# Kernel optimization log

Hardware: AMD Instinct MI355X
Metric: run time of the kernel (lower is better)

The kernel has to match this reference:

```python
import jax, jax.numpy as jnp
import numpy as np

N_HEADS = 4
SIGMA = 6.0
T_IN = 12
T_TOTAL = 24


def setup_inputs() -> dict:
    key = jax.random.key(0)
    k1, k2, k3, k4, k5 = jax.random.split(key, 5)
    B, T, N, C, K = 16, T_IN, 5000, 4, 16
    x = jax.random.normal(k1, (B, T, N, C), dtype=jnp.float32)
    dists = jax.random.uniform(k2, (N, K), dtype=jnp.float32) * 10.0  # kNN distances
    neighbors = jax.random.randint(k3, (N, K), 0, N)                  # kNN indices
    d_in = T * N_HEADS                   # 48
    d_out = T_TOTAL - T_IN               # 12
    W = jax.random.normal(k4, (d_in, d_out), dtype=jnp.float32) * (1.0 / np.sqrt(d_in))
    b = jax.random.normal(k5, (d_out,), dtype=jnp.float32) * 0.01
    return {"x": x, "dists": dists, "W": W, "b": b, "neighbors": neighbors}


def reference(x, dists, W, b, neighbors):
    B, T, N, C = x.shape
    H = N_HEADS
    # lambda_h = h/H for h = 1..H
    lam = jnp.arange(1, H + 1, dtype=x.dtype) / H                     # [H]
    # weights[n,k,h] = exp(-d_{nk}^2 * lam_h / sigma^2)
    w = jnp.exp(-(dists ** 2)[:, :, None] * lam / (SIGMA ** 2))       # [N,K,H]
    # gather neighbor features: [B,T,N,K,C]
    xg = x[:, :, neighbors, :]
    # distance-weighted aggregation over neighbors -> [B,T,N,H,C]
    agg = jnp.einsum('btnkc,nkh->btnhc', xg, w)
    # permute (0,2,4,1,3) -> [B,N,C,T,H], flatten last two -> [B,N,C,T*H]
    feat = jnp.transpose(agg, (0, 2, 4, 1, 3)).reshape(B, N, C, T * H)
    # shrink: Linear + ReLU -> [B,N,C,T_TOTAL-T]
    y = jax.nn.relu(feat @ W + b)
    # -> [B, T_TOTAL-T, N, C]
    y = jnp.transpose(y, (0, 3, 1, 2))
    return jnp.concatenate([x, y], axis=1)                            # [B,T_TOTAL,N,C]
```

## Files before the change

### kernel.cpp

```cpp
#include <hip/hip_runtime.h>

#define Bz 16
#define Tin 12
#define Ttot 24
#define NN 5000
#define Cc 4
#define KK 16
#define HH 4
#define OO 12
#define TH 48
#define G  8
#define JJ 24

typedef float f32x4 __attribute__((ext_vector_type(4)));
__device__ __forceinline__ void nt_store4(float4* p, float4 v) {
    f32x4 t; t.x = v.x; t.y = v.y; t.z = v.z; t.w = v.w;
    __builtin_nontemporal_store(t, (f32x4*)p);
}

#define K1_NB 64
#define K1_BT 24

__global__ __launch_bounds__(256) void transpose_kernel(
    const float4* __restrict__ x4,
    float4* __restrict__ xT2)
{
    __shared__ float4 tile[K1_BT][K1_NB + 1];
    const int bid = blockIdx.x;
    const int g   = bid & 7;
    const int n0  = (bid >> 3) * K1_NB;
    const int bt0 = g * K1_BT;
    const int rem = min(K1_NB, NN - n0);
    const int tid = threadIdx.x;

    #pragma unroll
    for (int r = 0; r < (K1_NB * K1_BT) / 256; r++) {
        int tau = r * 256 + tid;
        int j = tau / K1_NB;
        int i = tau % K1_NB;
        if (i < rem)
            tile[j][i] = x4[(size_t)(bt0 + j) * NN + n0 + i];
    }
    __syncthreads();

    #pragma unroll
    for (int r = 0; r < (K1_NB * K1_BT) / 256; r++) {
        int tau = r * 256 + tid;
        int i = tau / K1_BT;
        int j = tau - i * K1_BT;
        if (i < rem)
            xT2[((size_t)g * NN + n0 + i) * JJ + j] = tile[j][i];
    }
}

#define NPB 8
#define FST 5
#define FSB 61
#define FSN 123

__global__ __launch_bounds__(192) void gnn_main_kernel(
    const float4* __restrict__ x4,
    const float4* __restrict__ xT2,
    const float* __restrict__ dists,
    const float* __restrict__ W,
    const float* __restrict__ bias,
    const int*   __restrict__ nbrs,
    float4* __restrict__ out4)
{
    __shared__ float4 feat[NPB * FSN];
    __shared__ float4 w4_s[NPB][KK];
    __shared__ float  W_s[TH * OO];
    __shared__ float  bias_s[OO];
    __shared__ int    nbr_s[NPB][KK];

    const int bid = blockIdx.x;
    const int g   = bid & 7;
    const int n0  = (bid >> 3) * NPB;
    const int tid = threadIdx.x;

    for (int i = tid; i < TH * OO; i += 192) W_s[i] = W[i];
    if (tid < OO) bias_s[tid] = bias[tid];
    if (tid < NPB * KK) {
        int nl = tid >> 4, k = tid & 15;
        nbr_s[nl][k] = nbrs[(n0 + nl) * KK + k];
        float d = dists[(n0 + nl) * KK + k];
        float e = -(d * d) * (1.0f / 144.0f);
        float4 wv;
        wv.x = expf(e);
        wv.y = expf(2.0f * e);
        wv.z = expf(3.0f * e);
        wv.w = expf(4.0f * e);
        w4_s[nl][k] = wv;
    }

    {
        const int j  = tid >> 3;
        const int nl = tid & 7;
        const int bt = g * JJ + j;
        const int b  = bt / Tin, t = bt - b * Tin;
        float4 v = x4[(size_t)bt * NN + n0 + nl];
        nt_store4(&out4[(size_t)(b * Ttot + t) * NN + n0 + nl], v);
    }
    __syncthreads();

    {
        const int nl  = tid / JJ;
        const int j   = tid - nl * JJ;
        const int b_l = j / Tin;
        const int t   = j - b_l * Tin;
        const float4* xg = xT2 + (size_t)g * NN * JJ;

        float4 a0 = {0,0,0,0}, a1 = {0,0,0,0}, a2 = {0,0,0,0}, a3 = {0,0,0,0};
        #pragma unroll
        for (int k = 0; k < KK; k++) {
            float4 xv = xg[(size_t)nbr_s[nl][k] * JJ + j];
            float4 wv = w4_s[nl][k];
            a0.x += wv.x * xv.x; a0.y += wv.x * xv.y; a0.z += wv.x * xv.z; a0.w += wv.x * xv.w;
            a1.x += wv.y * xv.x; a1.y += wv.y * xv.y; a1.z += wv.y * xv.z; a1.w += wv.y * xv.w;
            a2.x += wv.z * xv.x; a2.y += wv.z * xv.y; a2.z += wv.z * xv.z; a2.w += wv.z * xv.w;
            a3.x += wv.w * xv.x; a3.y += wv.w * xv.y; a3.z += wv.w * xv.z; a3.w += wv.w * xv.w;
        }
        const int base = nl * FSN + b_l * FSB + t * FST;
        feat[base + 0] = a0;
        feat[base + 1] = a1;
        feat[base + 2] = a2;
        feat[base + 3] = a3;
    }
    __syncthreads();

    {
        const int nl  = tid & 7;
        const int bo  = tid >> 3;
        const int b_l = bo / OO;
        const int o   = bo - b_l * OO;
        const float bz = bias_s[o];
        float4 acc = {bz, bz, bz, bz};
        const int fbase = nl * FSN + b_l * FSB;
        #pragma unroll
        for (int t = 0; t < Tin; t++) {
            #pragma unroll
            for (int h = 0; h < HH; h++) {
                float  wv = W_s[(t * HH + h) * OO + o];
                float4 f  = feat[fbase + t * FST + h];
                acc.x += wv * f.x; acc.y += wv * f.y;
                acc.z += wv * f.z; acc.w += wv * f.w;
            }
        }
        acc.x = fmaxf(acc.x, 0.0f); acc.y = fmaxf(acc.y, 0.0f);
        acc.z = fmaxf(acc.z, 0.0f); acc.w = fmaxf(acc.w, 0.0f);
        const int b = g * 2 + b_l;
        nt_store4(&out4[(size_t)(b * Ttot + Tin + o) * NN + n0 + nl], acc);
    }
}

extern "C" void kernel_launch(void* const* d_in, const int* in_sizes, int n_in,
                              void* d_out, int out_size, void* d_ws, size_t ws_size,
                              hipStream_t stream) {
    const float* x     = (const float*)d_in[0];
    const float* dists = (const float*)d_in[1];
    const float* W     = (const float*)d_in[2];
    const float* bias  = (const float*)d_in[3];
    const int*   nbrs  = (const int*)d_in[4];
    float4* out4 = (float4*)d_out;
    float4* xT2  = (float4*)d_ws;

    const int ntiles = (NN + K1_NB - 1) / K1_NB;
    hipLaunchKernelGGL(transpose_kernel, dim3(ntiles * G), dim3(256), 0, stream,
                       (const float4*)x, xT2);

    hipLaunchKernelGGL(gnn_main_kernel, dim3((NN / NPB) * G), dim3(192), 0, stream,
                       (const float4*)x, (const float4*)xT2,
                       dists, W, bias, nbrs, out4);
}
```

Measured before the change: 106.1 us.

## Fuse transpose and main pass into one persistent cooperative kernel with grid sync

```diff
diff --git a/kernel.cpp b/kernel.cpp
--- a/kernel.cpp
+++ b/kernel.cpp
@@ -1,10 +1,12 @@
 #include <hip/hip_runtime.h>
+#include <hip/hip_cooperative_groups.h>
+
+namespace cg = cooperative_groups;
 
 #define Bz 16
 #define Tin 12
 #define Ttot 24
 #define NN 5000
-#define Cc 4
 #define KK 16
 #define HH 4
 #define OO 12
@@ -12,87 +14,201 @@
 #define G  8
 #define JJ 24
 
+#define BPG 128
+#define NPB 8
+#define GPG 625
+#define TNB 40
+#define NT  125
+
+#define FST 5
+#define FSB 61
+#define FSN 122
+
+#define OFF_W4   16000
+#define OFF_NBR  18048
+#define OFF_WS   18560
+#define OFF_BIAS 20864
+#define SMEM_BYTES 20928
+
 typedef float f32x4 __attribute__((ext_vector_type(4)));
 __device__ __forceinline__ void nt_store4(float4* p, float4 v) {
     f32x4 t; t.x = v.x; t.y = v.y; t.z = v.z; t.w = v.w;
     __builtin_nontemporal_store(t, (f32x4*)p);
 }
 
-#define K1_NB 64
-#define K1_BT 24
-
-__global__ __launch_bounds__(256) void transpose_kernel(
+__global__ __launch_bounds__(256, 4) void gnn_fused_kernel(
     const float4* __restrict__ x4,
-    float4* __restrict__ xT2)
-{
-    __shared__ float4 tile[K1_BT][K1_NB + 1];
-    const int bid = blockIdx.x;
-    const int g   = bid & 7;
-    const int n0  = (bid >> 3) * K1_NB;
-    const int bt0 = g * K1_BT;
-    const int rem = min(K1_NB, NN - n0);
-    const int tid = threadIdx.x;
-
-    #pragma unroll
-    for (int r = 0; r < (K1_NB * K1_BT) / 256; r++) {
-        int tau = r * 256 + tid;
-        int j = tau / K1_NB;
-        int i = tau % K1_NB;
-        if (i < rem)
-            tile[j][i] = x4[(size_t)(bt0 + j) * NN + n0 + i];
-    }
-    __syncthreads();
-
-    #pragma unroll
-    for (int r = 0; r < (K1_NB * K1_BT) / 256; r++) {
-        int tau = r * 256 + tid;
-        int i = tau / K1_BT;
-        int j = tau - i * K1_BT;
-        if (i < rem)
-            xT2[((size_t)g * NN + n0 + i) * JJ + j] = tile[j][i];
-    }
-}
-
-#define NPB 8
-#define FST 5
-#define FSB 61
-#define FSN 123
-
-__global__ __launch_bounds__(192) void gnn_main_kernel(
-    const float4* __restrict__ x4,
-    const float4* __restrict__ xT2,
+    float4* __restrict__ xT2,
     const float* __restrict__ dists,
     const float* __restrict__ W,
     const float* __restrict__ bias,
     const int*   __restrict__ nbrs,
     float4* __restrict__ out4)
 {
-    __shared__ float4 feat[NPB * FSN];
-    __shared__ float4 w4_s[NPB][KK];
-    __shared__ float  W_s[TH * OO];
-    __shared__ float  bias_s[OO];
-    __shared__ int    nbr_s[NPB][KK];
-
+    __shared__ __align__(16) unsigned char smem[SMEM_BYTES];
+    float4* feat   = (float4*)smem;
+    float4 (*tile)[TNB + 1] = (float4(*)[TNB + 1])smem;
+    float4* w4_s   = (float4*)(smem + OFF_W4);
+    int*    nbr_s  = (int*)  (smem + OFF_NBR);
+    float*  W_s    = (float*)(smem + OFF_WS);
+    float*  bias_s = (float*)(smem + OFF_BIAS);
+
+    const int bid  = blockIdx.x;
+    const int g    = bid & 7;
+    const int bidg = bid >> 3;
+    const int tid  = threadIdx.x;
+
+    for (int idx = bidg * 256 + tid; idx < JJ * NN; idx += BPG * 256) {
+        int j  = idx / NN;
+        int n  = idx - j * NN;
+        int bt = g * JJ + j;
+        int b  = bt / Tin, t = bt - b * Tin;
+        float4 v = x4[(size_t)bt * NN + n];
+        nt_store4(&out4[(size_t)(b * Ttot + t) * NN + n], v);
+    }
+    if (bidg < NT) {
+        const int n0 = bidg * TNB;
+        for (int tau = tid; tau < TNB * JJ; tau += 256) {
+            int jj = tau / TNB;
+            int ii = tau % TNB;
+            tile[jj][ii] = x4[(size_t)(g * JJ + jj) * NN + n0 + ii];
+        }
+        __syncthreads();
+        for (int tau = tid; tau < TNB * JJ; tau += 256) {
+            int i = tau / JJ;
+            int j = tau % JJ;
+            xT2[((size_t)g * NN + n0 + i) * JJ + j] = tile[j][i];
+        }
+    }
+
+    cg::this_grid().sync();
+
+    for (int i = tid; i < TH * OO; i += 256) W_s[i] = W[i];
+    if (tid < OO) bias_s[tid] = bias[tid];
+
+    const float4* xg = xT2 + (size_t)g * NN * JJ;
+
+    for (int grp = bidg; grp < GPG; grp += BPG) {
+        const int n0 = grp * NPB;
+
+        if (tid < NPB * KK) {
+            int nl = tid >> 4, k = tid & 15;
+            nbr_s[nl * KK + k] = nbrs[(n0 + nl) * KK + k];
+            float d = dists[(n0 + nl) * KK + k];
+            float e = -(d * d) * (1.0f / 144.0f);
+            float4 wv;
+            wv.x = expf(e);
+            wv.y = expf(2.0f * e);
+            wv.z = expf(3.0f * e);
+            wv.w = expf(4.0f * e);
+            w4_s[nl * KK + k] = wv;
+        }
+        __syncthreads();
+
+        if (tid < NPB * JJ) {
+            const int nl  = tid / JJ;
+            const int j   = tid - nl * JJ;
+            const int b_l = j / Tin;
+            const int t   = j - b_l * Tin;
+            float4 a0 = {0,0,0,0}, a1 = {0,0,0,0}, a2 = {0,0,0,0}, a3 = {0,0,0,0};
+            #pragma unroll
+            for (int k = 0; k < KK; k++) {
+                float4 xv = xg[(size_t)nbr_s[nl * KK + k] * JJ + j];
+                float4 wv = w4_s[nl * KK + k];
+                a0.x += wv.x * xv.x; a0.y += wv.x * xv.y; a0.z += wv.x * xv.z; a0.w += wv.x * xv.w;
+                a1.x += wv.y * xv.x; a1.y += wv.y * xv.y; a1.z += wv.y * xv.z; a1.w += wv.y * xv.w;
+                a2.x += wv.z * xv.x; a2.y += wv.z * xv.y; a2.z += wv.z * xv.z; a2.w += wv.z * xv.w;
+                a3.x += wv.w * xv.x; a3.y += wv.w * xv.y; a3.z += wv.w * xv.z; a3.w += wv.w * xv.w;
+            }
+            const int base = nl * FSN + b_l * FSB + t * FST;
+            feat[base + 0] = a0;
+            feat[base + 1] = a1;
+            feat[base + 2] = a2;
+            feat[base + 3] = a3;
+        }
+        __syncthreads();
+
+        if (tid < NPB * JJ) {
+            const int nl  = tid & 7;
+            const int bo  = tid >> 3;
+            const int b_l = bo / OO;
+            const int o   = bo - b_l * OO;
+            const float bz = bias_s[o];
+            float4 acc = {bz, bz, bz, bz};
+            const int fbase = nl * FSN + b_l * FSB;
+            #pragma unroll
+            for (int t = 0; t < Tin; t++) {
+                #pragma unroll
+                for (int h = 0; h < HH; h++) {
+                    float  wv = W_s[(t * HH + h) * OO + o];
+                    float4 f  = feat[fbase + t * FST + h];
+                    acc.x += wv * f.x; acc.y += wv * f.y;
+                    acc.z += wv * f.z; acc.w += wv * f.w;
+                }
+            }
+            acc.x = fmaxf(acc.x, 0.0f); acc.y = fmaxf(acc.y, 0.0f);
+            acc.z = fmaxf(acc.z, 0.0f); acc.w = fmaxf(acc.w, 0.0f);
+            const int b = g * 2 + b_l;
+            nt_store4(&out4[(size_t)(b * Ttot + Tin + o) * NN + n0 + nl], acc);
+        }
+    }
+}
+
+#define K1_NB 64
+
+__global__ __launch_bounds__(256) void transpose_kernel(
+    const float4* __restrict__ x4, float4* __restrict__ xT2)
+{
+    __shared__ float4 tileA[JJ][K1_NB + 1];
+    const int bid = blockIdx.x;
+    const int g   = bid & 7;
+    const int n0  = (bid >> 3) * K1_NB;
+    const int rem = min(K1_NB, NN - n0);
+    const int tid = threadIdx.x;
+    #pragma unroll
+    for (int r = 0; r < (K1_NB * JJ) / 256; r++) {
+        int tau = r * 256 + tid;
+        int j = tau / K1_NB, i = tau % K1_NB;
+        if (i < rem)
+            tileA[j][i] = x4[(size_t)(g * JJ + j) * NN + n0 + i];
+    }
+    __syncthreads();
+    #pragma unroll
+    for (int r = 0; r < (K1_NB * JJ) / 256; r++) {
+        int tau = r * 256 + tid;
+        int i = tau / JJ, j = tau - i * JJ;
+        if (i < rem)
+            xT2[((size_t)g * NN + n0 + i) * JJ + j] = tileA[j][i];
+    }
+}
+
+__global__ __launch_bounds__(192) void gnn_main_kernel(
+    const float4* __restrict__ x4, const float4* __restrict__ xT2,
+    const float* __restrict__ dists, const float* __restrict__ W,
+    const float* __restrict__ bias, const int* __restrict__ nbrs,
+    float4* __restrict__ out4)
+{
+    __shared__ float4 featB[NPB * 123];
+    __shared__ float4 w4B[NPB][KK];
+    __shared__ float  WB[TH * OO];
+    __shared__ float  biasB[OO];
+    __shared__ int    nbrB[NPB][KK];
     const int bid = blockIdx.x;
     const int g   = bid & 7;
     const int n0  = (bid >> 3) * NPB;
     const int tid = threadIdx.x;
-
-    for (int i = tid; i < TH * OO; i += 192) W_s[i] = W[i];
-    if (tid < OO) bias_s[tid] = bias[tid];
+    for (int i = tid; i < TH * OO; i += 192) WB[i] = W[i];
+    if (tid < OO) biasB[tid] = bias[tid];
     if (tid < NPB * KK) {
         int nl = tid >> 4, k = tid & 15;
-        nbr_s[nl][k] = nbrs[(n0 + nl) * KK + k];
+        nbrB[nl][k] = nbrs[(n0 + nl) * KK + k];
         float d = dists[(n0 + nl) * KK + k];
         float e = -(d * d) * (1.0f / 144.0f);
         float4 wv;
-        wv.x = expf(e);
-        wv.y = expf(2.0f * e);
-        wv.z = expf(3.0f * e);
-        wv.w = expf(4.0f * e);
-        w4_s[nl][k] = wv;
-    }
-
+        wv.x = expf(e); wv.y = expf(2.0f * e);
+        wv.z = expf(3.0f * e); wv.w = expf(4.0f * e);
+        w4B[nl][k] = wv;
+    }
     {
         const int j  = tid >> 3;
         const int nl = tid & 7;
@@ -102,50 +218,44 @@
         nt_store4(&out4[(size_t)(b * Ttot + t) * NN + n0 + nl], v);
     }
     __syncthreads();
-
     {
         const int nl  = tid / JJ;
         const int j   = tid - nl * JJ;
         const int b_l = j / Tin;
         const int t   = j - b_l * Tin;
         const float4* xg = xT2 + (size_t)g * NN * JJ;
-
         float4 a0 = {0,0,0,0}, a1 = {0,0,0,0}, a2 = {0,0,0,0}, a3 = {0,0,0,0};
         #pragma unroll
         for (int k = 0; k < KK; k++) {
-            float4 xv = xg[(size_t)nbr_s[nl][k] * JJ + j];
-            float4 wv = w4_s[nl][k];
+            float4 xv = xg[(size_t)nbrB[nl][k] * JJ + j];
+            float4 wv = w4B[nl][k];
             a0.x += wv.x * xv.x; a0.y += wv.x * xv.y; a0.z += wv.x * xv.z; a0.w += wv.x * xv.w;
             a1.x += wv.y * xv.x; a1.y += wv.y * xv.y; a1.z += wv.y * xv.z; a1.w += wv.y * xv.w;
             a2.x += wv.z * xv.x; a2.y += wv.z * xv.y; a2.z += wv.z * xv.z; a2.w += wv.z * xv.w;
             a3.x += wv.w * xv.x; a3.y += wv.w * xv.y; a3.z += wv.w * xv.z; a3.w += wv.w * xv.w;
         }
-        const int base = nl * FSN + b_l * FSB + t * FST;
-        feat[base + 0] = a0;
-        feat[base + 1] = a1;
-        feat[base + 2] = a2;
-        feat[base + 3] = a3;
+        const int base = nl * 123 + b_l * FSB + t * FST;
+        featB[base + 0] = a0; featB[base + 1] = a1;
+        featB[base + 2] = a2; featB[base + 3] = a3;
     }
     __syncthreads();
-
     {
         const int nl  = tid & 7;
         const int bo  = tid >> 3;
         const int b_l = bo / OO;
         const int o   = bo - b_l * OO;
-        const float bz = bias_s[o];
+        const float bz = biasB[o];
         float4 acc = {bz, bz, bz, bz};
-        const int fbase = nl * FSN + b_l * FSB;
+        const int fbase = nl * 123 + b_l * FSB;
         #pragma unroll
-        for (int t = 0; t < Tin; t++) {
+        for (int t = 0; t < Tin; t++)
             #pragma unroll
             for (int h = 0; h < HH; h++) {
-                float  wv = W_s[(t * HH + h) * OO + o];
-                float4 f  = feat[fbase + t * FST + h];
+                float  wv = WB[(t * HH + h) * OO + o];
+                float4 f  = featB[fbase + t * FST + h];
                 acc.x += wv * f.x; acc.y += wv * f.y;
                 acc.z += wv * f.z; acc.w += wv * f.w;
             }
-        }
         acc.x = fmaxf(acc.x, 0.0f); acc.y = fmaxf(acc.y, 0.0f);
         acc.z = fmaxf(acc.z, 0.0f); acc.w = fmaxf(acc.w, 0.0f);
         const int b = g * 2 + b_l;
@@ -156,19 +266,26 @@
 extern "C" void kernel_launch(void* const* d_in, const int* in_sizes, int n_in,
                               void* d_out, int out_size, void* d_ws, size_t ws_size,
                               hipStream_t stream) {
-    const float* x     = (const float*)d_in[0];
-    const float* dists = (const float*)d_in[1];
-    const float* W     = (const float*)d_in[2];
-    const float* bias  = (const float*)d_in[3];
-    const int*   nbrs  = (const int*)d_in[4];
+    const float4* x4    = (const float4*)d_in[0];
+    const float*  dists = (const float*)d_in[1];
+    const float*  W     = (const float*)d_in[2];
+    const float*  bias  = (const float*)d_in[3];
+    const int*    nbrs  = (const int*)d_in[4];
     float4* out4 = (float4*)d_out;
     float4* xT2  = (float4*)d_ws;
 
-    const int ntiles = (NN + K1_NB - 1) / K1_NB;
-    hipLaunchKernelGGL(transpose_kernel, dim3(ntiles * G), dim3(256), 0, stream,
-                       (const float4*)x, xT2);
-
-    hipLaunchKernelGGL(gnn_main_kernel, dim3((NN / NPB) * G), dim3(192), 0, stream,
-                       (const float4*)x, (const float4*)xT2,
-                       dists, W, bias, nbrs, out4);
-}
+    void* args[] = { (void*)&x4, (void*)&xT2, (void*)&dists, (void*)&W,
+                     (void*)&bias, (void*)&nbrs, (void*)&out4 };
+    hipError_t err = hipLaunchCooperativeKernel(
+        (const void*)gnn_fused_kernel, dim3(G * BPG), dim3(256),
+        args, 0, stream);
+
+    if (err != hipSuccess) {
+        const int ntiles = (NN + K1_NB - 1) / K1_NB;
+        hipLaunchKernelGGL(transpose_kernel, dim3(ntiles * G), dim3(256), 0,
+                           stream, x4, xT2);
+        hipLaunchKernelGGL(gnn_main_kernel, dim3((NN / NPB) * G), dim3(192), 0,
+                           stream, x4, (const float4*)xT2,
+                           dists, W, bias, nbrs, out4);
+    }
+}
```

Measured after the change: 247.6 us. 133% more time.
